# Performance work log

Hardware: AMD Instinct MI355X
Metric: run time of the kernel (lower is better)

## Reference

```python
import jax, jax.numpy as jnp
import numpy as np

N_SRNA = 20000
N_MRNA = 100000
HID = 128
E_S2M = 1_000_000
E_M2M = 2_000_000
E_LBL = 500_000
N_LAYERS = 2


def setup_inputs() -> dict:
    key = jax.random.key(0)
    ks = jax.random.split(key, 20)
    s = 0.05
    inp = {
        # edge lists (rev edge types are flips, derived inside reference)
        "s2m_src": jax.random.randint(ks[0], (E_S2M,), 0, N_SRNA),
        "s2m_dst": jax.random.randint(ks[1], (E_S2M,), 0, N_MRNA),
        "m2m_src": jax.random.randint(ks[2], (E_M2M,), 0, N_MRNA),
        "m2m_dst": jax.random.randint(ks[3], (E_M2M,), 0, N_MRNA),
        "label_src": jax.random.randint(ks[4], (E_LBL,), 0, N_SRNA),
        "label_dst": jax.random.randint(ks[5], (E_LBL,), 0, N_MRNA),
        # embeddings (node_id is arange over all nodes -> identity lookup)
        "srna_emb": jax.random.normal(ks[6], (N_SRNA, HID), jnp.float32),
        "mrna_emb": jax.random.normal(ks[7], (N_MRNA, HID), jnp.float32),
        # per-layer stacked params. SAGEConv: out = lin_l(mean_agg)+lin_r(x_dst)
        "sage_s2m_Wl": jax.random.normal(ks[8], (N_LAYERS, HID, HID), jnp.float32) * s,
        "sage_s2m_bl": jnp.zeros((N_LAYERS, HID), jnp.float32),
        "sage_s2m_Wr": jax.random.normal(ks[9], (N_LAYERS, HID, HID), jnp.float32) * s,
        "sage_rev_Wl": jax.random.normal(ks[10], (N_LAYERS, HID, HID), jnp.float32) * s,
        "sage_rev_bl": jnp.zeros((N_LAYERS, HID), jnp.float32),
        "sage_rev_Wr": jax.random.normal(ks[11], (N_LAYERS, HID, HID), jnp.float32) * s,
        # GCNConv: out = propagate(norm, x @ W) + b
        "gcn_m2m_W": jax.random.normal(ks[12], (N_LAYERS, HID, HID), jnp.float32) * s,
        "gcn_m2m_b": jnp.zeros((N_LAYERS, HID), jnp.float32),
        "gcn_rev_W": jax.random.normal(ks[13], (N_LAYERS, HID, HID), jnp.float32) * s,
        "gcn_rev_b": jnp.zeros((N_LAYERS, HID), jnp.float32),
    }
    return inp


def _sage(x_src, x_dst, src, dst, n_dst, Wl, bl, Wr):
    # PyG SAGEConv (aggr='mean', root_weight=True): lin_l(mean_msg) + lin_r(x_dst)
    agg = jax.ops.segment_sum(x_src[src], dst, num_segments=n_dst)  # [n_dst, h]
    cnt = jax.ops.segment_sum(jnp.ones((src.shape[0],), x_src.dtype), dst,
                              num_segments=n_dst)
    agg = agg / jnp.maximum(cnt, 1.0)[:, None]
    return agg @ Wl + bl + x_dst @ Wr


def _gcn(x, src, dst, n, W, b):
    # PyG GCNConv: add self-loops, sym-normalize, x @ W, propagate, + bias
    xw = x @ W  # [n, h]
    deg = jax.ops.segment_sum(jnp.ones((src.shape[0],), x.dtype), dst,
                              num_segments=n) + 1.0  # +1 self-loop
    dinv = jax.lax.rsqrt(deg)
    norm = dinv[src] * dinv[dst]  # [E]
    out = jax.ops.segment_sum(norm[:, None] * xw[src], dst, num_segments=n)
    out = out + (dinv * dinv)[:, None] * xw  # self-loop term
    return out + b


def reference(s2m_src, s2m_dst, m2m_src, m2m_dst, label_src, label_dst,
              srna_emb, mrna_emb,
              sage_s2m_Wl, sage_s2m_bl, sage_s2m_Wr,
              sage_rev_Wl, sage_rev_bl, sage_rev_Wr,
              gcn_m2m_W, gcn_m2m_b, gcn_rev_W, gcn_rev_b):
    x_s, x_m = srna_emb, mrna_emb
    for l in range(N_LAYERS):
        # HeteroConv aggr='sum' over edge types per dst node type
        m_new = _sage(x_s, x_m, s2m_src, s2m_dst, N_MRNA,
                      sage_s2m_Wl[l], sage_s2m_bl[l], sage_s2m_Wr[l])
        m_new = m_new + _gcn(x_m, m2m_src, m2m_dst, N_MRNA,
                             gcn_m2m_W[l], gcn_m2m_b[l])
        m_new = m_new + _gcn(x_m, m2m_dst, m2m_src, N_MRNA,
                             gcn_rev_W[l], gcn_rev_b[l])  # rev_similar = flip
        s_new = _sage(x_m, x_s, s2m_dst, s2m_src, N_SRNA,
                      sage_rev_Wl[l], sage_rev_bl[l], sage_rev_Wr[l])
        x_s, x_m = jax.nn.relu(s_new), jax.nn.relu(m_new)
    # Classifier: dot product over labeled (srna, mrna) pairs
    return (x_s[label_src] * x_m[label_dst]).sum(axis=-1)
```

## Files before the change

kernel.cpp:

```cpp
#include <hip/hip_runtime.h>
#include <hip/hip_fp16.h>

#define NS 20000
#define NM 100000
#define H  128
#define ES 1000000
#define EM 2000000
#define EL 500000

#define SH_M 7
#define SH_S 6
#define NB_SD 782
#define NB_SS 313
#define NB_MD 782
#define NB_MS 782
#define CAP_SD 1664
#define CAP_SS 3904
#define CAP_MD 3200
#define CAP_MS 3200
#define MAXCAP 3904
#define CHUNK 4096
#define B_SD ((ES + CHUNK - 1) / CHUNK)
#define B_SS ((ES + CHUNK - 1) / CHUNK)
#define B_MD ((EM + CHUNK - 1) / CHUNK)
#define B_MS ((EM + CHUNK - 1) / CHUNK)
#define VAL_MASK 0x1FFFF

typedef _Float16 half8 __attribute__((ext_vector_type(8)));
typedef float floatx4 __attribute__((ext_vector_type(4)));

__global__ __launch_bounds__(256) void place1_sorted(
        const int* __restrict__ s2m_src, const int* __restrict__ s2m_dst,
        const int* __restrict__ m2m_src, const int* __restrict__ m2m_dst,
        int* __restrict__ bc,
        unsigned int* __restrict__ p_sd, unsigned int* __restrict__ p_ss,
        unsigned int* __restrict__ p_md, unsigned int* __restrict__ p_ms) {
    __shared__ unsigned int rec[CHUNK];
    __shared__ unsigned short eb[CHUNK];
    __shared__ int cnt[1024];
    __shared__ int gbase[1024];

    int b = blockIdx.x;
    const int *keys, *vals; int shift, cap, E, bcoff; unsigned int* pp;
    int cb;
    if (b < B_SD)                    { cb = b;                      keys = s2m_dst; vals = s2m_src; shift = SH_M; cap = CAP_SD; E = ES; bcoff = 0;     pp = p_sd; }
    else if (b < B_SD+B_SS)          { cb = b - B_SD;               keys = s2m_src; vals = s2m_dst; shift = SH_S; cap = CAP_SS; E = ES; bcoff = 16384; pp = p_ss; }
    else if (b < B_SD+B_SS+B_MD)     { cb = b - B_SD - B_SS;        keys = m2m_dst; vals = m2m_src; shift = SH_M; cap = CAP_MD; E = EM; bcoff = 32768; pp = p_md; }
    else                             { cb = b - B_SD - B_SS - B_MD; keys = m2m_src; vals = m2m_dst; shift = SH_M; cap = CAP_MS; E = EM; bcoff = 49152; pp = p_ms; }
    int* bcp = bc + bcoff;

    int t = threadIdx.x;
    int e0 = cb * CHUNK;
    int nv = E - e0; if (nv > CHUNK) nv = CHUNK;

    for (int i = t; i < nv; i += 256) {
        int k = keys[e0 + i];
        int v = vals[e0 + i];
        int bkt = k >> shift;
        rec[i] = ((unsigned int)(k - (bkt << shift)) << 17) | (unsigned int)v;
        eb[i] = (unsigned short)bkt;
    }
#pragma unroll
    for (int j = 0; j < 4; ++j) cnt[t * 4 + j] = 0;
    __syncthreads();
    for (int i = t; i < nv; i += 256) atomicAdd(&cnt[eb[i]], 1);
    __syncthreads();
#pragma unroll
    for (int j = 0; j < 4; ++j) {
        int bk = t * 4 + j;
        int c = cnt[bk];
        if (c > 0) {
            gbase[bk] = atomicAdd(&bcp[bk << 4], c);
            cnt[bk] = 0;
        }
    }
    __syncthreads();
    for (int i = t; i < nv; i += 256) {
        int bk = eb[i];
        int pos = atomicAdd(&cnt[bk], 1);
        int o = gbase[bk] + pos;
        if (o < cap) pp[(size_t)bk * cap + o] = rec[i];
    }
}

__global__ __launch_bounds__(256) void place2_fused(
        const int* __restrict__ bc,
        const unsigned int* __restrict__ p_sd, const unsigned int* __restrict__ p_ss,
        const unsigned int* __restrict__ p_md, const unsigned int* __restrict__ p_ms,
        int* __restrict__ adj_sd, int* __restrict__ adj_ss,
        int* __restrict__ adj_md, int* __restrict__ adj_ms,
        int* __restrict__ off_sd, int* __restrict__ off_ss,
        int* __restrict__ off_md, int* __restrict__ off_ms,
        int* __restrict__ cnt_sd, int* __restrict__ cnt_ss,
        int* __restrict__ cnt_md, int* __restrict__ cnt_ms) {
    __shared__ unsigned int lp[MAXCAP];
    __shared__ int hist[128], cur[128], sbuf[128];
    int b = blockIdx.x;
    int c, lb;
    if (b < NB_SD)                    { c = 0; lb = b; }
    else if (b < NB_SD+NB_SS)         { c = 1; lb = b - NB_SD; }
    else if (b < NB_SD+NB_SS+NB_MD)   { c = 2; lb = b - NB_SD - NB_SS; }
    else                              { c = 3; lb = b - NB_SD - NB_SS - NB_MD; }
    const unsigned int* pp; int *adj, *offp, *cntp; int shift, cap, n;
    switch (c) {
    case 0:  pp = p_sd; adj = adj_sd; offp = off_sd; cntp = cnt_sd; shift = SH_M; cap = CAP_SD; n = NM; break;
    case 1:  pp = p_ss; adj = adj_ss; offp = off_ss; cntp = cnt_ss; shift = SH_S; cap = CAP_SS; n = NS; break;
    case 2:  pp = p_md; adj = adj_md; offp = off_md; cntp = cnt_md; shift = SH_M; cap = CAP_MD; n = NM; break;
    default: pp = p_ms; adj = adj_ms; offp = off_ms; cntp = cnt_ms; shift = SH_M; cap = CAP_MS; n = NM; break;
    }
    int t = threadIdx.x;
    int k = bc[c * 16384 + (lb << 4)];
    if (k > cap) k = cap;
    int base = lb << shift;
    int npb = 1 << shift;
    int bb = lb * cap;
    for (int i = t; i < k; i += 256) lp[i] = pp[(size_t)lb * cap + i];
    if (t < npb) hist[t] = 0;
    __syncthreads();
    for (int i = t; i < k; i += 256) atomicAdd(&hist[lp[i] >> 17], 1);
    __syncthreads();
    int v = (t < npb) ? hist[t] : 0;
    if (t < 128) sbuf[t] = v;
    __syncthreads();
    for (int d = 1; d < 128; d <<= 1) {
        int x = 0;
        if (t >= d && t < 128) x = sbuf[t - d];
        __syncthreads();
        if (t >= d && t < 128) sbuf[t] += x;
        __syncthreads();
    }
    if (t < npb) {
        int excl = sbuf[t] - v;
        cur[t] = excl;
        int node = base + t;
        if (node < n) { offp[node] = bb + excl; cntp[node] = v; }
    }
    __syncthreads();
    for (int i = t; i < k; i += 256) {
        unsigned int p = lp[i];
        int pos = atomicAdd(&cur[p >> 17], 1);
        adj[(size_t)bb + pos] = (int)(p & VAL_MASK);
    }
}

__global__ void finalize_scales(const int* __restrict__ c_md, const int* __restrict__ c_ms,
                                float* __restrict__ dvf, float* __restrict__ dvr) {
    int i = blockIdx.x * blockDim.x + threadIdx.x;
    if (i < NM) {
        dvf[i] = rsqrtf((float)c_md[i] + 1.0f);
        dvr[i] = rsqrtf((float)c_ms[i] + 1.0f);
    }
}

__global__ void to_half(const float* __restrict__ in, __half* __restrict__ out,
                        long long n4) {
    long long i = (long long)blockIdx.x * blockDim.x + threadIdx.x;
    if (i >= n4) return;
    float4 v = *(const float4*)&in[i * 4];
    __half2 h0 = __floats2half2_rn(v.x, v.y);
    __half2 h1 = __floats2half2_rn(v.z, v.w);
    __half2* o = (__half2*)&out[i * 4];
    o[0] = h0; o[1] = h1;
}

__global__ void prep_w(const float* __restrict__ w0, const float* __restrict__ w1,
                       const float* __restrict__ w2, const float* __restrict__ w3,
                       const float* __restrict__ w4, const float* __restrict__ w5,
                       __half* __restrict__ out) {
    int idx = blockIdx.x * 256 + threadIdx.x;
    if (idx >= 12 * H * H) return;
    int mat = idx / (H * H);
    int rem = idx % (H * H);
    int n = rem / H;
    int k = rem % H;
    const float* base;
    switch (mat >> 1) {
    case 0: base = w0; break; case 1: base = w1; break; case 2: base = w2; break;
    case 3: base = w3; break; case 4: base = w4; break; default: base = w5; break;
    }
    base += (size_t)(mat & 1) * H * H;
    out[(size_t)mat * H * H + (size_t)n * H + k] = __float2half(base[(size_t)k * H + n]);
}

__device__ __forceinline__ float4 ldh4(const __half* __restrict__ X, long long idx) {
    float2 raw = *(const float2*)(X + idx);
    __half2 h0 = *(__half2*)&raw.x;
    __half2 h1 = *(__half2*)&raw.y;
    float2 fa = __half22float2(h0);
    float2 fb = __half22float2(h1);
    return make_float4(fa.x, fa.y, fb.x, fb.y);
}

__device__ __forceinline__ void gacc_plain(const __half* __restrict__ X,
                                           const int* __restrict__ adj,
                                           int o, int k, int c, float (&acc)[8]) {
    int j = 0;
    for (; j + 8 <= k; j += 8) {
        int s0 = adj[o+j+0], s1 = adj[o+j+1], s2 = adj[o+j+2], s3 = adj[o+j+3];
        int s4 = adj[o+j+4], s5 = adj[o+j+5], s6 = adj[o+j+6], s7 = adj[o+j+7];
        half8 v0 = *(const half8*)(X + (size_t)s0 * H + c);
        half8 v1 = *(const half8*)(X + (size_t)s1 * H + c);
        half8 v2 = *(const half8*)(X + (size_t)s2 * H + c);
        half8 v3 = *(const half8*)(X + (size_t)s3 * H + c);
        half8 v4 = *(const half8*)(X + (size_t)s4 * H + c);
        half8 v5 = *(const half8*)(X + (size_t)s5 * H + c);
        half8 v6 = *(const half8*)(X + (size_t)s6 * H + c);
        half8 v7 = *(const half8*)(X + (size_t)s7 * H + c);
#pragma unroll
        for (int i = 0; i < 8; ++i)
            acc[i] += (float)v0[i] + (float)v1[i] + (float)v2[i] + (float)v3[i]
                    + (float)v4[i] + (float)v5[i] + (float)v6[i] + (float)v7[i];
    }
    for (; j + 4 <= k; j += 4) {
        int s0 = adj[o+j+0], s1 = adj[o+j+1], s2 = adj[o+j+2], s3 = adj[o+j+3];
        half8 v0 = *(const half8*)(X + (size_t)s0 * H + c);
        half8 v1 = *(const half8*)(X + (size_t)s1 * H + c);
        half8 v2 = *(const half8*)(X + (size_t)s2 * H + c);
        half8 v3 = *(const half8*)(X + (size_t)s3 * H + c);
#pragma unroll
        for (int i = 0; i < 8; ++i)
            acc[i] += (float)v0[i] + (float)v1[i] + (float)v2[i] + (float)v3[i];
    }
    for (; j < k; ++j) {
        int s = adj[o + j];
        half8 v = *(const half8*)(X + (size_t)s * H + c);
#pragma unroll
        for (int i = 0; i < 8; ++i) acc[i] += (float)v[i];
    }
}

__device__ __forceinline__ void gacc_weighted(const __half* __restrict__ X,
                                              const int* __restrict__ adj,
                                              const float* __restrict__ dinv,
                                              int o, int k, int c, float (&acc)[8]) {
    int j = 0;
    for (; j + 8 <= k; j += 8) {
        int s0 = adj[o+j+0], s1 = adj[o+j+1], s2 = adj[o+j+2], s3 = adj[o+j+3];
        int s4 = adj[o+j+4], s5 = adj[o+j+5], s6 = adj[o+j+6], s7 = adj[o+j+7];
        float d0 = dinv[s0], d1 = dinv[s1], d2 = dinv[s2], d3 = dinv[s3];
        float d4 = dinv[s4], d5 = dinv[s5], d6 = dinv[s6], d7 = dinv[s7];
        half8 v0 = *(const half8*)(X + (size_t)s0 * H + c);
        half8 v1 = *(const half8*)(X + (size_t)s1 * H + c);
        half8 v2 = *(const half8*)(X + (size_t)s2 * H + c);
        half8 v3 = *(const half8*)(X + (size_t)s3 * H + c);
        half8 v4 = *(const half8*)(X + (size_t)s4 * H + c);
        half8 v5 = *(const half8*)(X + (size_t)s5 * H + c);
        half8 v6 = *(const half8*)(X + (size_t)s6 * H + c);
        half8 v7 = *(const half8*)(X + (size_t)s7 * H + c);
#pragma unroll
        for (int i = 0; i < 8; ++i)
            acc[i] += d0 * (float)v0[i] + d1 * (float)v1[i] + d2 * (float)v2[i] + d3 * (float)v3[i]
                    + d4 * (float)v4[i] + d5 * (float)v5[i] + d6 * (float)v6[i] + d7 * (float)v7[i];
    }
    for (; j + 4 <= k; j += 4) {
        int s0 = adj[o+j+0], s1 = adj[o+j+1], s2 = adj[o+j+2], s3 = adj[o+j+3];
        float d0 = dinv[s0], d1 = dinv[s1], d2 = dinv[s2], d3 = dinv[s3];
        half8 v0 = *(const half8*)(X + (size_t)s0 * H + c);
        half8 v1 = *(const half8*)(X + (size_t)s1 * H + c);
        half8 v2 = *(const half8*)(X + (size_t)s2 * H + c);
        half8 v3 = *(const half8*)(X + (size_t)s3 * H + c);
#pragma unroll
        for (int i = 0; i < 8; ++i)
            acc[i] += d0 * (float)v0[i] + d1 * (float)v1[i] + d2 * (float)v2[i] + d3 * (float)v3[i];
    }
    for (; j < k; ++j) {
        int s = adj[o + j];
        float ds = dinv[s];
        half8 v = *(const half8*)(X + (size_t)s * H + c);
#pragma unroll
        for (int i = 0; i < 8; ++i) acc[i] += ds * (float)v[i];
    }
}

__device__ __forceinline__ void sth8(__half* __restrict__ X, size_t idx, const float (&a)[8]) {
    half8 h;
#pragma unroll
    for (int i = 0; i < 8; ++i) h[i] = (_Float16)a[i];
    *(half8*)(X + idx) = h;
}

__global__ void mega_gather(const __half* __restrict__ xs16, const __half* __restrict__ xm16,
                            const int* __restrict__ off_sd, const int* __restrict__ cnt_sd,
                            const int* __restrict__ adj_sd,
                            const int* __restrict__ off_md, const int* __restrict__ cnt_md,
                            const int* __restrict__ adj_md,
                            const int* __restrict__ off_ms, const int* __restrict__ cnt_ms,
                            const int* __restrict__ adj_ms,
                            const int* __restrict__ off_ss, const int* __restrict__ cnt_ss,
                            const int* __restrict__ adj_ss,
                            const float* __restrict__ dvf, const float* __restrict__ dvr,
                            __half* __restrict__ SA, __half* __restrict__ Qf,
                            __half* __restrict__ Qr, __half* __restrict__ Qs) {
    long long gid = (long long)blockIdx.x * blockDim.x + threadIdx.x;
    int g = (int)(gid >> 4);
    int c = ((int)gid & 15) * 8;
    float acc[8] = {0.f, 0.f, 0.f, 0.f, 0.f, 0.f, 0.f, 0.f};
    if (g < NM) {
        int k = cnt_sd[g];
        gacc_plain(xs16, adj_sd, off_sd[g], k, c, acc);
        float ic = 1.0f / fmaxf((float)k, 1.0f);
#pragma unroll
        for (int i = 0; i < 8; ++i) acc[i] *= ic;
        sth8(SA, (size_t)g * H + c, acc);
    } else if (g < 2 * NM) {
        int r = g - NM;
        gacc_weighted(xm16, adj_md, dvf, off_md[r], cnt_md[r], c, acc);
        float dd = dvf[r];
        float s2 = dd * dd;
        half8 self = *(const half8*)(xm16 + (size_t)r * H + c);
#pragma unroll
        for (int i = 0; i < 8; ++i) acc[i] = dd * acc[i] + s2 * (float)self[i];
        sth8(Qf, (size_t)r * H + c, acc);
    } else if (g < 3 * NM) {
        int r = g - 2 * NM;
        gacc_weighted(xm16, adj_ms, dvr, off_ms[r], cnt_ms[r], c, acc);
        float dd = dvr[r];
        float s2 = dd * dd;
        half8 self = *(const half8*)(xm16 + (size_t)r * H + c);
#pragma unroll
        for (int i = 0; i < 8; ++i) acc[i] = dd * acc[i] + s2 * (float)self[i];
        sth8(Qr, (size_t)r * H + c, acc);
    } else if (g < 3 * NM + NS) {
        int r = g - 3 * NM;
        int k = cnt_ss[r];
        gacc_plain(xm16, adj_ss, off_ss[r], k, c, acc);
        float ic = 1.0f / fmaxf((float)k, 1.0f);
#pragma unroll
        for (int i = 0; i < 8; ++i) acc[i] *= ic;
        sth8(Qs, (size_t)r * H + c, acc);
    }
}

__device__ __forceinline__ void mfma_stage(const __half* __restrict__ A,
                                           const __half* __restrict__ Wt,
                                           int gr, int M, int nlo, int quad,
                                           floatx4 (&acc)[8]) {
#pragma unroll
    for (int k0 = 0; k0 < 128; k0 += 32) {
        half8 a;
        if (gr < M) {
            a = *(const half8*)(A + (size_t)gr * H + k0 + quad * 8);
        } else {
            float4 z = make_float4(0.f, 0.f, 0.f, 0.f);
            a = *(half8*)&z;
        }
#pragma unroll
        for (int t = 0; t < 8; ++t) {
            half8 b = *(const half8*)(Wt + (size_t)(t * 16 + nlo) * H + k0 + quad * 8);
            acc[t] = __builtin_amdgcn_mfma_f32_16x16x32_f16(a, b, acc[t], 0, 0, 0);
        }
    }
}

__global__ __launch_bounds__(256) void mega_gemm_mfma(
        const __half* __restrict__ SA, const __half* __restrict__ Qf,
        const __half* __restrict__ Qr, const __half* __restrict__ xm_in,
        const __half* __restrict__ Qs, const __half* __restrict__ xs_in,
        const __half* __restrict__ wbuf,
        const float* __restrict__ bl, const float* __restrict__ gb,
        const float* __restrict__ grb, const float* __restrict__ bls,
        __half* __restrict__ xm_out, __half* __restrict__ xs_out,
        int MBLK, int layer)
{
    const int tid = threadIdx.x;
    const int w = tid >> 6;
    const int lane = tid & 63;
    const int quad = lane >> 4;
    const int nlo = lane & 15;
    const size_t HH = (size_t)H * H;

    floatx4 acc[8];
#pragma unroll
    for (int t = 0; t < 8; ++t) {
        acc[t][0] = 0.f; acc[t][1] = 0.f; acc[t][2] = 0.f; acc[t][3] = 0.f;
    }

    if ((int)blockIdx.x < MBLK) {
        const int bm = blockIdx.x * 64 + w * 16;
        const int gr = bm + nlo;
        mfma_stage(SA,    wbuf + (0 * 2 + layer) * HH, gr, NM, nlo, quad, acc);
        mfma_stage(xm_in, wbuf + (1 * 2 + layer) * HH, gr, NM, nlo, quad, acc);
        mfma_stage(Qf,    wbuf + (2 * 2 + layer) * HH, gr, NM, nlo, quad, acc);
        mfma_stage(Qr,    wbuf + (3 * 2 + layer) * HH, gr, NM, nlo, quad, acc);
#pragma unroll
        for (int t = 0; t < 8; ++t) {
            int col = t * 16 + nlo;
            float bias = bl[col] + gb[col] + grb[col];
#pragma unroll
            for (int i = 0; i < 4; ++i) {
                int r = bm + quad * 4 + i;
                if (r < NM)
                    xm_out[(size_t)r * H + col] = __float2half(fmaxf(acc[t][i] + bias, 0.f));
            }
        }
    } else {
        const int bm = ((int)blockIdx.x - MBLK) * 64 + w * 16;
        const int gr = bm + nlo;
        mfma_stage(Qs,    wbuf + (4 * 2 + layer) * HH, gr, NS, nlo, quad, acc);
        mfma_stage(xs_in, wbuf + (5 * 2 + layer) * HH, gr, NS, nlo, quad, acc);
#pragma unroll
        for (int t = 0; t < 8; ++t) {
            int col = t * 16 + nlo;
            float bias = bls[col];
#pragma unroll
            for (int i = 0; i < 4; ++i) {
                int r = bm + quad * 4 + i;
                if (r < NS)
                    xs_out[(size_t)r * H + col] = __float2half(fmaxf(acc[t][i] + bias, 0.f));
            }
        }
    }
}

__global__ void classify(const __half* __restrict__ xs16, const __half* __restrict__ xm16,
                         const int* __restrict__ ls, const int* __restrict__ ld,
                         float* __restrict__ out, int P) {
    long long gid = (long long)blockIdx.x * blockDim.x + threadIdx.x;
    int p = (int)(gid >> 5);
    if (p >= P) return;
    int lane = (int)gid & 31;
    int a = ls[p], b = ld[p];
    float4 u = ldh4(xs16, (long long)a * H + lane * 4);
    float4 v = ldh4(xm16, (long long)b * H + lane * 4);
    float s = u.x * v.x + u.y * v.y + u.z * v.z + u.w * v.w;
    for (int off = 16; off > 0; off >>= 1) s += __shfl_down(s, off, 32);
    if (lane == 0) out[p] = s;
}

extern "C" void kernel_launch(void* const* d_in, const int* in_sizes, int n_in,
                              void* d_out, int out_size, void* d_ws, size_t ws_size,
                              hipStream_t stream) {
    const int* s2m_src = (const int*)d_in[0];
    const int* s2m_dst = (const int*)d_in[1];
    const int* m2m_src = (const int*)d_in[2];
    const int* m2m_dst = (const int*)d_in[3];
    const int* lbl_src = (const int*)d_in[4];
    const int* lbl_dst = (const int*)d_in[5];
    const float* s_emb = (const float*)d_in[6];
    const float* m_emb = (const float*)d_in[7];
    const float* Wl_s2m = (const float*)d_in[8];
    const float* bl_s2m = (const float*)d_in[9];
    const float* Wr_s2m = (const float*)d_in[10];
    const float* Wl_rev = (const float*)d_in[11];
    const float* bl_rev = (const float*)d_in[12];
    const float* Wr_rev = (const float*)d_in[13];
    const float* gW  = (const float*)d_in[14];
    const float* gb  = (const float*)d_in[15];
    const float* grW = (const float*)d_in[16];
    const float* grb = (const float*)d_in[17];

    __half* hws = (__half*)d_ws;
    size_t ho = 0;
    __half* xm16_a = hws + ho; ho += (size_t)NM * H;
    __half* xm16_b = hws + ho; ho += (size_t)NM * H;
    __half* xs16_a = hws + ho; ho += (size_t)NS * H;
    __half* xs16_b = hws + ho; ho += (size_t)NS * H;
    __half* SA = hws + ho; ho += (size_t)NM * H;
    __half* Qf = hws + ho; ho += (size_t)NM * H;
    __half* Qr = hws + ho; ho += (size_t)NM * H;
    __half* Qs = hws + ho; ho += (size_t)NS * H;
    __half* wbuf = hws + ho; ho += (size_t)12 * H * H;

    float* fws = (float*)(hws + ho);
    size_t fo = 0;
    float* dvf = fws + fo; fo += NM;
    float* dvr = fws + fo; fo += NM;

    int* ip = (int*)(fws + fo);
    size_t io = 0;
    int* off_sd = ip + io; io += NM;
    int* off_ss = ip + io; io += NS;
    int* off_md = ip + io; io += NM;
    int* off_ms = ip + io; io += NM;
    int* cnt_sd = ip + io; io += NM;
    int* cnt_ss = ip + io; io += NS;
    int* cnt_md = ip + io; io += NM;
    int* cnt_ms = ip + io; io += NM;
    int* bc     = ip + io; io += 4 * 16384;
    int* adj_sd = ip + io; io += NB_SD * CAP_SD;
    int* adj_ss = ip + io; io += NB_SS * CAP_SS;
    int* adj_md = ip + io; io += NB_MD * CAP_MD;
    int* adj_ms = ip + io; io += NB_MS * CAP_MS;

    unsigned int* p_sd = (unsigned int*)SA;
    unsigned int* p_ss = p_sd + (size_t)NB_SD * CAP_SD;
    unsigned int* p_md = p_ss + (size_t)NB_SS * CAP_SS;
    unsigned int* p_ms = p_md + (size_t)NB_MD * CAP_MD;

    const int bM = (NM + 255) / 256;

    hipMemsetAsync(bc, 0, 4 * 16384 * sizeof(int), stream);
    place1_sorted<<<B_SD + B_SS + B_MD + B_MS, 256, 0, stream>>>(
        s2m_src, s2m_dst, m2m_src, m2m_dst, bc, p_sd, p_ss, p_md, p_ms);
    place2_fused<<<NB_SD + NB_SS + NB_MD + NB_MS, 256, 0, stream>>>(
        bc, p_sd, p_ss, p_md, p_ms,
        adj_sd, adj_ss, adj_md, adj_ms,
        off_sd, off_ss, off_md, off_ms,
        cnt_sd, cnt_ss, cnt_md, cnt_ms);
    finalize_scales<<<bM, 256, 0, stream>>>(cnt_md, cnt_ms, dvf, dvr);

    const long long n4m = (long long)NM * H / 4;
    const long long n4s = (long long)NS * H / 4;
    to_half<<<(int)((n4m + 255) / 256), 256, 0, stream>>>(m_emb, xm16_a, n4m);
    to_half<<<(int)((n4s + 255) / 256), 256, 0, stream>>>(s_emb, xs16_a, n4s);
    prep_w<<<(12 * H * H + 255) / 256, 256, 0, stream>>>(
        Wl_s2m, Wr_s2m, gW, grW, Wl_rev, Wr_rev, wbuf);

    const int gMega = (int)(((long long)(3 * NM + NS) * 16 + 255) / 256);
    const int MBLK = (NM + 63) / 64;
    const int SBLK = (NS + 63) / 64;

    const __half* xin_m = xm16_a;
    const __half* xin_s = xs16_a;
    __half* xout_m = xm16_b;
    __half* xout_s = xs16_b;

    for (int l = 0; l < 2; ++l) {
        const size_t bo = (size_t)l * H;

        mega_gather<<<gMega, 256, 0, stream>>>(xin_s, xin_m,
                                               off_sd, cnt_sd, adj_sd,
                                               off_md, cnt_md, adj_md,
                                               off_ms, cnt_ms, adj_ms,
                                               off_ss, cnt_ss, adj_ss,
                                               dvf, dvr, SA, Qf, Qr, Qs);

        mega_gemm_mfma<<<MBLK + SBLK, 256, 0, stream>>>(
            SA, Qf, Qr, xin_m, Qs, xin_s, wbuf,
            bl_s2m + bo, gb + bo, grb + bo, bl_rev + bo,
            xout_m, xout_s, MBLK, l);

        const __half* tm = xin_m; xin_m = xout_m; xout_m = (__half*)tm;
        const __half* ts = xin_s; xin_s = xout_s; xout_s = (__half*)ts;
    }

    classify<<<(int)(((long long)EL * 32 + 255) / 256), 256, 0, stream>>>(
        xin_s, xin_m, lbl_src, lbl_dst, (float*)d_out, EL);
}
```

Baseline: 961.1 us.

## Fuse neighbor gather with MFMA GEMM per layer and merge prep kernels

The gather and GEMM stages of each layer are merged into one kernel. Each block aggregates 16 destination rows into LDS tiles and then runs the MFMA projection directly from LDS, so the SA/Qf/Qr/Qs intermediates no longer make a round trip through global memory. The three prep kernels (half conversion, weight transpose, degree scales) are also merged into a single launch. In exchange, each thread now does three serial gathers for mRNA rows, the GEMM tile shrinks to 16 rows, and the B weight fragments are reloaded from global memory by every block.

```diff
diff --git a/kernel.cpp b/kernel.cpp
--- a/kernel.cpp
+++ b/kernel.cpp
@@ -25,6 +25,15 @@
 #define B_MD ((EM + CHUNK - 1) / CHUNK)
 #define B_MS ((EM + CHUNK - 1) / CHUNK)
 #define VAL_MASK 0x1FFFF
+
+#define MB_M (NM / 16)
+#define MB_S (NS / 16)
+#define APAD 136
+
+#define PB_M 12500
+#define PB_S 2500
+#define PB_W 768
+#define PB_F 391
 
 typedef _Float16 half8 __attribute__((ext_vector_type(8)));
 typedef float floatx4 __attribute__((ext_vector_type(4)));
@@ -143,52 +152,50 @@
     }
 }
 
-__global__ void finalize_scales(const int* __restrict__ c_md, const int* __restrict__ c_ms,
-                                float* __restrict__ dvf, float* __restrict__ dvr) {
-    int i = blockIdx.x * blockDim.x + threadIdx.x;
-    if (i < NM) {
-        dvf[i] = rsqrtf((float)c_md[i] + 1.0f);
-        dvr[i] = rsqrtf((float)c_ms[i] + 1.0f);
-    }
-}
-
-__global__ void to_half(const float* __restrict__ in, __half* __restrict__ out,
-                        long long n4) {
-    long long i = (long long)blockIdx.x * blockDim.x + threadIdx.x;
-    if (i >= n4) return;
-    float4 v = *(const float4*)&in[i * 4];
-    __half2 h0 = __floats2half2_rn(v.x, v.y);
-    __half2 h1 = __floats2half2_rn(v.z, v.w);
-    __half2* o = (__half2*)&out[i * 4];
-    o[0] = h0; o[1] = h1;
-}
-
-__global__ void prep_w(const float* __restrict__ w0, const float* __restrict__ w1,
-                       const float* __restrict__ w2, const float* __restrict__ w3,
-                       const float* __restrict__ w4, const float* __restrict__ w5,
-                       __half* __restrict__ out) {
-    int idx = blockIdx.x * 256 + threadIdx.x;
-    if (idx >= 12 * H * H) return;
-    int mat = idx / (H * H);
-    int rem = idx % (H * H);
-    int n = rem / H;
-    int k = rem % H;
-    const float* base;
-    switch (mat >> 1) {
-    case 0: base = w0; break; case 1: base = w1; break; case 2: base = w2; break;
-    case 3: base = w3; break; case 4: base = w4; break; default: base = w5; break;
-    }
-    base += (size_t)(mat & 1) * H * H;
-    out[(size_t)mat * H * H + (size_t)n * H + k] = __float2half(base[(size_t)k * H + n]);
-}
-
-__device__ __forceinline__ float4 ldh4(const __half* __restrict__ X, long long idx) {
-    float2 raw = *(const float2*)(X + idx);
-    __half2 h0 = *(__half2*)&raw.x;
-    __half2 h1 = *(__half2*)&raw.y;
-    float2 fa = __half22float2(h0);
-    float2 fb = __half22float2(h1);
-    return make_float4(fa.x, fa.y, fb.x, fb.y);
+__global__ __launch_bounds__(256) void prep_all(
+        const float* __restrict__ m_emb, const float* __restrict__ s_emb,
+        const float* __restrict__ w0, const float* __restrict__ w1,
+        const float* __restrict__ w2, const float* __restrict__ w3,
+        const float* __restrict__ w4, const float* __restrict__ w5,
+        const int* __restrict__ c_md, const int* __restrict__ c_ms,
+        __half* __restrict__ xm16, __half* __restrict__ xs16,
+        __half* __restrict__ wbuf, float* __restrict__ dvf, float* __restrict__ dvr) {
+    int b = blockIdx.x;
+    int t = threadIdx.x;
+    if (b < PB_M) {
+        long long i = (long long)b * 256 + t;
+        float4 v = *(const float4*)&m_emb[i * 4];
+        __half2 h0 = __floats2half2_rn(v.x, v.y);
+        __half2 h1 = __floats2half2_rn(v.z, v.w);
+        __half2* o = (__half2*)&xm16[i * 4];
+        o[0] = h0; o[1] = h1;
+    } else if (b < PB_M + PB_S) {
+        long long i = (long long)(b - PB_M) * 256 + t;
+        float4 v = *(const float4*)&s_emb[i * 4];
+        __half2 h0 = __floats2half2_rn(v.x, v.y);
+        __half2 h1 = __floats2half2_rn(v.z, v.w);
+        __half2* o = (__half2*)&xs16[i * 4];
+        o[0] = h0; o[1] = h1;
+    } else if (b < PB_M + PB_S + PB_W) {
+        int idx = (b - PB_M - PB_S) * 256 + t;
+        int mat = idx / (H * H);
+        int rem = idx % (H * H);
+        int n = rem / H;
+        int k = rem % H;
+        const float* base;
+        switch (mat >> 1) {
+        case 0: base = w0; break; case 1: base = w1; break; case 2: base = w2; break;
+        case 3: base = w3; break; case 4: base = w4; break; default: base = w5; break;
+        }
+        base += (size_t)(mat & 1) * H * H;
+        wbuf[(size_t)mat * H * H + (size_t)n * H + k] = __float2half(base[(size_t)k * H + n]);
+    } else {
+        int i = (b - PB_M - PB_S - PB_W) * 256 + t;
+        if (i < NM) {
+            dvf[i] = rsqrtf((float)c_md[i] + 1.0f);
+            dvr[i] = rsqrtf((float)c_ms[i] + 1.0f);
+        }
+    }
 }
 
 __device__ __forceinline__ void gacc_plain(const __half* __restrict__ X,
@@ -272,144 +279,138 @@
     }
 }
 
-__device__ __forceinline__ void sth8(__half* __restrict__ X, size_t idx, const float (&a)[8]) {
+__device__ __forceinline__ void st_lds8(__half* p, const float (&a)[8]) {
     half8 h;
 #pragma unroll
     for (int i = 0; i < 8; ++i) h[i] = (_Float16)a[i];
-    *(half8*)(X + idx) = h;
-}
-
-__global__ void mega_gather(const __half* __restrict__ xs16, const __half* __restrict__ xm16,
-                            const int* __restrict__ off_sd, const int* __restrict__ cnt_sd,
-                            const int* __restrict__ adj_sd,
-                            const int* __restrict__ off_md, const int* __restrict__ cnt_md,
-                            const int* __restrict__ adj_md,
-                            const int* __restrict__ off_ms, const int* __restrict__ cnt_ms,
-                            const int* __restrict__ adj_ms,
-                            const int* __restrict__ off_ss, const int* __restrict__ cnt_ss,
-                            const int* __restrict__ adj_ss,
-                            const float* __restrict__ dvf, const float* __restrict__ dvr,
-                            __half* __restrict__ SA, __half* __restrict__ Qf,
-                            __half* __restrict__ Qr, __half* __restrict__ Qs) {
-    long long gid = (long long)blockIdx.x * blockDim.x + threadIdx.x;
-    int g = (int)(gid >> 4);
-    int c = ((int)gid & 15) * 8;
-    float acc[8] = {0.f, 0.f, 0.f, 0.f, 0.f, 0.f, 0.f, 0.f};
-    if (g < NM) {
-        int k = cnt_sd[g];
-        gacc_plain(xs16, adj_sd, off_sd[g], k, c, acc);
-        float ic = 1.0f / fmaxf((float)k, 1.0f);
-#pragma unroll
-        for (int i = 0; i < 8; ++i) acc[i] *= ic;
-        sth8(SA, (size_t)g * H + c, acc);
-    } else if (g < 2 * NM) {
-        int r = g - NM;
-        gacc_weighted(xm16, adj_md, dvf, off_md[r], cnt_md[r], c, acc);
-        float dd = dvf[r];
-        float s2 = dd * dd;
-        half8 self = *(const half8*)(xm16 + (size_t)r * H + c);
-#pragma unroll
-        for (int i = 0; i < 8; ++i) acc[i] = dd * acc[i] + s2 * (float)self[i];
-        sth8(Qf, (size_t)r * H + c, acc);
-    } else if (g < 3 * NM) {
-        int r = g - 2 * NM;
-        gacc_weighted(xm16, adj_ms, dvr, off_ms[r], cnt_ms[r], c, acc);
-        float dd = dvr[r];
-        float s2 = dd * dd;
-        half8 self = *(const half8*)(xm16 + (size_t)r * H + c);
-#pragma unroll
-        for (int i = 0; i < 8; ++i) acc[i] = dd * acc[i] + s2 * (float)self[i];
-        sth8(Qr, (size_t)r * H + c, acc);
-    } else if (g < 3 * NM + NS) {
-        int r = g - 3 * NM;
-        int k = cnt_ss[r];
-        gacc_plain(xm16, adj_ss, off_ss[r], k, c, acc);
-        float ic = 1.0f / fmaxf((float)k, 1.0f);
-#pragma unroll
-        for (int i = 0; i < 8; ++i) acc[i] *= ic;
-        sth8(Qs, (size_t)r * H + c, acc);
-    }
-}
-
-__device__ __forceinline__ void mfma_stage(const __half* __restrict__ A,
-                                           const __half* __restrict__ Wt,
-                                           int gr, int M, int nlo, int quad,
-                                           floatx4 (&acc)[8]) {
-#pragma unroll
-    for (int k0 = 0; k0 < 128; k0 += 32) {
-        half8 a;
-        if (gr < M) {
-            a = *(const half8*)(A + (size_t)gr * H + k0 + quad * 8);
-        } else {
-            float4 z = make_float4(0.f, 0.f, 0.f, 0.f);
-            a = *(half8*)&z;
-        }
-#pragma unroll
-        for (int t = 0; t < 8; ++t) {
-            half8 b = *(const half8*)(Wt + (size_t)(t * 16 + nlo) * H + k0 + quad * 8);
-            acc[t] = __builtin_amdgcn_mfma_f32_16x16x32_f16(a, b, acc[t], 0, 0, 0);
-        }
-    }
-}
-
-__global__ __launch_bounds__(256) void mega_gemm_mfma(
-        const __half* __restrict__ SA, const __half* __restrict__ Qf,
-        const __half* __restrict__ Qr, const __half* __restrict__ xm_in,
-        const __half* __restrict__ Qs, const __half* __restrict__ xs_in,
+    *(half8*)p = h;
+}
+
+__global__ __launch_bounds__(256) void fused_layer(
+        const __half* __restrict__ xs_in, const __half* __restrict__ xm_in,
+        const int* __restrict__ off_sd, const int* __restrict__ cnt_sd, const int* __restrict__ adj_sd,
+        const int* __restrict__ off_md, const int* __restrict__ cnt_md, const int* __restrict__ adj_md,
+        const int* __restrict__ off_ms, const int* __restrict__ cnt_ms, const int* __restrict__ adj_ms,
+        const int* __restrict__ off_ss, const int* __restrict__ cnt_ss, const int* __restrict__ adj_ss,
+        const float* __restrict__ dvf, const float* __restrict__ dvr,
         const __half* __restrict__ wbuf,
         const float* __restrict__ bl, const float* __restrict__ gb,
         const float* __restrict__ grb, const float* __restrict__ bls,
-        __half* __restrict__ xm_out, __half* __restrict__ xs_out,
-        int MBLK, int layer)
+        __half* __restrict__ xm_out, __half* __restrict__ xs_out, int layer)
 {
-    const int tid = threadIdx.x;
-    const int w = tid >> 6;
-    const int lane = tid & 63;
-    const int quad = lane >> 4;
-    const int nlo = lane & 15;
+    __shared__ __half At[4][16][APAD];
+    const int t = threadIdx.x;
+    const int grp = t >> 4;
+    const int c = (t & 15) * 8;
     const size_t HH = (size_t)H * H;
-
-    floatx4 acc[8];
-#pragma unroll
-    for (int t = 0; t < 8; ++t) {
-        acc[t][0] = 0.f; acc[t][1] = 0.f; acc[t][2] = 0.f; acc[t][3] = 0.f;
-    }
-
-    if ((int)blockIdx.x < MBLK) {
-        const int bm = blockIdx.x * 64 + w * 16;
-        const int gr = bm + nlo;
-        mfma_stage(SA,    wbuf + (0 * 2 + layer) * HH, gr, NM, nlo, quad, acc);
-        mfma_stage(xm_in, wbuf + (1 * 2 + layer) * HH, gr, NM, nlo, quad, acc);
-        mfma_stage(Qf,    wbuf + (2 * 2 + layer) * HH, gr, NM, nlo, quad, acc);
-        mfma_stage(Qr,    wbuf + (3 * 2 + layer) * HH, gr, NM, nlo, quad, acc);
-#pragma unroll
-        for (int t = 0; t < 8; ++t) {
-            int col = t * 16 + nlo;
+    const bool isM = (int)blockIdx.x < MB_M;
+
+    if (isM) {
+        const int r = blockIdx.x * 16 + grp;
+        float acc[8] = {0.f,0.f,0.f,0.f,0.f,0.f,0.f,0.f};
+        int k = cnt_sd[r];
+        gacc_plain(xs_in, adj_sd, off_sd[r], k, c, acc);
+        float ic = 1.0f / fmaxf((float)k, 1.0f);
+#pragma unroll
+        for (int i = 0; i < 8; ++i) acc[i] *= ic;
+        st_lds8(&At[0][grp][c], acc);
+        half8 self = *(const half8*)(xm_in + (size_t)r * H + c);
+        *(half8*)&At[1][grp][c] = self;
+#pragma unroll
+        for (int i = 0; i < 8; ++i) acc[i] = 0.f;
+        gacc_weighted(xm_in, adj_md, dvf, off_md[r], cnt_md[r], c, acc);
+        float dd = dvf[r], s2 = dd * dd;
+#pragma unroll
+        for (int i = 0; i < 8; ++i) acc[i] = dd * acc[i] + s2 * (float)self[i];
+        st_lds8(&At[2][grp][c], acc);
+#pragma unroll
+        for (int i = 0; i < 8; ++i) acc[i] = 0.f;
+        gacc_weighted(xm_in, adj_ms, dvr, off_ms[r], cnt_ms[r], c, acc);
+        dd = dvr[r]; s2 = dd * dd;
+#pragma unroll
+        for (int i = 0; i < 8; ++i) acc[i] = dd * acc[i] + s2 * (float)self[i];
+        st_lds8(&At[3][grp][c], acc);
+        __syncthreads();
+        const int w = t >> 6, lane = t & 63, quad = lane >> 4, nlo = lane & 15;
+        floatx4 o0, o1;
+        o0[0]=0.f;o0[1]=0.f;o0[2]=0.f;o0[3]=0.f;
+        o1[0]=0.f;o1[1]=0.f;o1[2]=0.f;o1[3]=0.f;
+        const int t0 = 2 * w, t1 = 2 * w + 1;
+#pragma unroll
+        for (int seg = 0; seg < 4; ++seg) {
+            const __half* Wt = wbuf + (size_t)(seg * 2 + layer) * HH;
+#pragma unroll
+            for (int k0 = 0; k0 < 128; k0 += 32) {
+                half8 a = *(const half8*)&At[seg][nlo][k0 + quad * 8];
+                half8 b0 = *(const half8*)(Wt + (size_t)(t0 * 16 + nlo) * H + k0 + quad * 8);
+                half8 b1 = *(const half8*)(Wt + (size_t)(t1 * 16 + nlo) * H + k0 + quad * 8);
+                o0 = __builtin_amdgcn_mfma_f32_16x16x32_f16(a, b0, o0, 0, 0, 0);
+                o1 = __builtin_amdgcn_mfma_f32_16x16x32_f16(a, b1, o1, 0, 0, 0);
+            }
+        }
+        const int bm = blockIdx.x * 16;
+#pragma unroll
+        for (int u = 0; u < 2; ++u) {
+            floatx4 oo = u ? o1 : o0;
+            int col = (2 * w + u) * 16 + nlo;
             float bias = bl[col] + gb[col] + grb[col];
 #pragma unroll
             for (int i = 0; i < 4; ++i) {
-                int r = bm + quad * 4 + i;
-                if (r < NM)
-                    xm_out[(size_t)r * H + col] = __float2half(fmaxf(acc[t][i] + bias, 0.f));
+                int rr = bm + quad * 4 + i;
+                xm_out[(size_t)rr * H + col] = __float2half(fmaxf(oo[i] + bias, 0.f));
             }
         }
     } else {
-        const int bm = ((int)blockIdx.x - MBLK) * 64 + w * 16;
-        const int gr = bm + nlo;
-        mfma_stage(Qs,    wbuf + (4 * 2 + layer) * HH, gr, NS, nlo, quad, acc);
-        mfma_stage(xs_in, wbuf + (5 * 2 + layer) * HH, gr, NS, nlo, quad, acc);
-#pragma unroll
-        for (int t = 0; t < 8; ++t) {
-            int col = t * 16 + nlo;
+        const int blk = (int)blockIdx.x - MB_M;
+        const int r = blk * 16 + grp;
+        float acc[8] = {0.f,0.f,0.f,0.f,0.f,0.f,0.f,0.f};
+        int k = cnt_ss[r];
+        gacc_plain(xm_in, adj_ss, off_ss[r], k, c, acc);
+        float ic = 1.0f / fmaxf((float)k, 1.0f);
+#pragma unroll
+        for (int i = 0; i < 8; ++i) acc[i] *= ic;
+        st_lds8(&At[0][grp][c], acc);
+        *(half8*)&At[1][grp][c] = *(const half8*)(xs_in + (size_t)r * H + c);
+        __syncthreads();
+        const int w = t >> 6, lane = t & 63, quad = lane >> 4, nlo = lane & 15;
+        floatx4 o0, o1;
+        o0[0]=0.f;o0[1]=0.f;o0[2]=0.f;o0[3]=0.f;
+        o1[0]=0.f;o1[1]=0.f;o1[2]=0.f;o1[3]=0.f;
+        const int t0 = 2 * w, t1 = 2 * w + 1;
+#pragma unroll
+        for (int seg = 0; seg < 2; ++seg) {
+            const __half* Wt = wbuf + (size_t)((4 + seg) * 2 + layer) * HH;
+#pragma unroll
+            for (int k0 = 0; k0 < 128; k0 += 32) {
+                half8 a = *(const half8*)&At[seg][nlo][k0 + quad * 8];
+                half8 b0 = *(const half8*)(Wt + (size_t)(t0 * 16 + nlo) * H + k0 + quad * 8);
+                half8 b1 = *(const half8*)(Wt + (size_t)(t1 * 16 + nlo) * H + k0 + quad * 8);
+                o0 = __builtin_amdgcn_mfma_f32_16x16x32_f16(a, b0, o0, 0, 0, 0);
+                o1 = __builtin_amdgcn_mfma_f32_16x16x32_f16(a, b1, o1, 0, 0, 0);
+            }
+        }
+        const int bm = blk * 16;
+#pragma unroll
+        for (int u = 0; u < 2; ++u) {
+            floatx4 oo = u ? o1 : o0;
+            int col = (2 * w + u) * 16 + nlo;
             float bias = bls[col];
 #pragma unroll
             for (int i = 0; i < 4; ++i) {
-                int r = bm + quad * 4 + i;
-                if (r < NS)
-                    xs_out[(size_t)r * H + col] = __float2half(fmaxf(acc[t][i] + bias, 0.f));
+                int rr = bm + quad * 4 + i;
+                xs_out[(size_t)rr * H + col] = __float2half(fmaxf(oo[i] + bias, 0.f));
             }
         }
     }
+}
+
+__device__ __forceinline__ float4 ldh4(const __half* __restrict__ X, long long idx) {
+    float2 raw = *(const float2*)(X + idx);
+    __half2 h0 = *(__half2*)&raw.x;
+    __half2 h1 = *(__half2*)&raw.y;
+    float2 fa = __half22float2(h0);
+    float2 fb = __half22float2(h1);
+    return make_float4(fa.x, fa.y, fb.x, fb.y);
 }
 
 __global__ void classify(const __half* __restrict__ xs16, const __half* __restrict__ xm16,
@@ -455,10 +456,7 @@
     __half* xm16_b = hws + ho; ho += (size_t)NM * H;
     __half* xs16_a = hws + ho; ho += (size_t)NS * H;
     __half* xs16_b = hws + ho; ho += (size_t)NS * H;
-    __half* SA = hws + ho; ho += (size_t)NM * H;
-    __half* Qf = hws + ho; ho += (size_t)NM * H;
-    __half* Qr = hws + ho; ho += (size_t)NM * H;
-    __half* Qs = hws + ho; ho += (size_t)NS * H;
+    __half* scratch = hws + ho; ho += (size_t)(3 * NM + NS) * H;
     __half* wbuf = hws + ho; ho += (size_t)12 * H * H;
 
     float* fws = (float*)(hws + ho);
@@ -482,12 +480,10 @@
     int* adj_md = ip + io; io += NB_MD * CAP_MD;
     int* adj_ms = ip + io; io += NB_MS * CAP_MS;
 
-    unsigned int* p_sd = (unsigned int*)SA;
+    unsigned int* p_sd = (unsigned int*)scratch;
     unsigned int* p_ss = p_sd + (size_t)NB_SD * CAP_SD;
     unsigned int* p_md = p_ss + (size_t)NB_SS * CAP_SS;
     unsigned int* p_ms = p_md + (size_t)NB_MD * CAP_MD;
-
-    const int bM = (NM + 255) / 256;
 
     hipMemsetAsync(bc, 0, 4 * 16384 * sizeof(int), stream);
     place1_sorted<<<B_SD + B_SS + B_MD + B_MS, 256, 0, stream>>>(
@@ -497,18 +493,10 @@
         adj_sd, adj_ss, adj_md, adj_ms,
         off_sd, off_ss, off_md, off_ms,
         cnt_sd, cnt_ss, cnt_md, cnt_ms);
-    finalize_scales<<<bM, 256, 0, stream>>>(cnt_md, cnt_ms, dvf, dvr);
-
-    const long long n4m = (long long)NM * H / 4;
-    const long long n4s = (long long)NS * H / 4;
-    to_half<<<(int)((n4m + 255) / 256), 256, 0, stream>>>(m_emb, xm16_a, n4m);
-    to_half<<<(int)((n4s + 255) / 256), 256, 0, stream>>>(s_emb, xs16_a, n4s);
-    prep_w<<<(12 * H * H + 255) / 256, 256, 0, stream>>>(
-        Wl_s2m, Wr_s2m, gW, grW, Wl_rev, Wr_rev, wbuf);
-
-    const int gMega = (int)(((long long)(3 * NM + NS) * 16 + 255) / 256);
-    const int MBLK = (NM + 63) / 64;
-    const int SBLK = (NS + 63) / 64;
+
+    prep_all<<<PB_M + PB_S + PB_W + PB_F, 256, 0, stream>>>(
+        m_emb, s_emb, Wl_s2m, Wr_s2m, gW, grW, Wl_rev, Wr_rev,
+        cnt_md, cnt_ms, xm16_a, xs16_a, wbuf, dvf, dvr);
 
     const __half* xin_m = xm16_a;
     const __half* xin_s = xs16_a;
@@ -517,19 +505,15 @@
 
     for (int l = 0; l < 2; ++l) {
         const size_t bo = (size_t)l * H;
-
-        mega_gather<<<gMega, 256, 0, stream>>>(xin_s, xin_m,
-                                               off_sd, cnt_sd, adj_sd,
-                                               off_md, cnt_md, adj_md,
-                                               off_ms, cnt_ms, adj_ms,
-                                               off_ss, cnt_ss, adj_ss,
-                                               dvf, dvr, SA, Qf, Qr, Qs);
-
-        mega_gemm_mfma<<<MBLK + SBLK, 256, 0, stream>>>(
-            SA, Qf, Qr, xin_m, Qs, xin_s, wbuf,
+        fused_layer<<<MB_M + MB_S, 256, 0, stream>>>(
+            xin_s, xin_m,
+            off_sd, cnt_sd, adj_sd,
+            off_md, cnt_md, adj_md,
+            off_ms, cnt_ms, adj_ms,
+            off_ss, cnt_ss, adj_ss,
+            dvf, dvr, wbuf,
             bl_s2m + bo, gb + bo, grb + bo, bl_rev + bo,
-            xout_m, xout_s, MBLK, l);
-
+            xout_m, xout_s, l);
         const __half* tm = xin_m; xin_m = xout_m; xout_m = (__half*)tm;
         const __half* ts = xin_s; xin_s = xout_s; xout_s = (__half*)ts;
     }
```

After: 844.5 us. -12.1%, faster.
